# Optimization experiments

Hardware: AMD Instinct MI355X
Metric: run time of the kernel (lower is better)

Reference implementation:

```python
import jax, jax.numpy as jnp
import numpy as np

N, C, T, V = 64, 128, 64, 25   # batch, channels (2*base_channel), frames, joints
MAX_ORDER = 6                  # Adams-Bashforth order used by ODESolver
# _BASHFORTH_COEFFICIENTS[6] / _DIVISOR[6]
_AB_NUM = [4277.0, -7923.0, 9982.0, -7298.0, 2877.0, -475.0]
_AB_DEN = 1440.0


def _init_pe(length, d_model):
    # Sinusoidal positional encoding, shaped [1, d_model, length, 1] like ODEFunc.init_pe
    position = np.arange(length, dtype=np.float32)[:, None]
    div_term = np.exp(np.arange(0, d_model, 2, dtype=np.float32) * -(np.log(10000.0) / d_model))
    pe = np.zeros((length, d_model), dtype=np.float32)
    pe[:, 0::2] = np.sin(position * div_term)
    pe[:, 1::2] = np.cos(position * div_term)
    return jnp.asarray(pe.T[None, :, :, None])


def setup_inputs() -> dict:
    key = jax.random.key(0)
    ks = jax.random.split(key, 8)
    h = jax.random.normal(ks[0], (N, C, T, V), dtype=jnp.float32)
    # replaces torch.rand(B,1,1,1) teacher-forcing draws, one per integration step
    mask_rand = jax.random.uniform(ks[1], (T - MAX_ORDER, N, 1, 1, 1), dtype=jnp.float32)
    # normalized adjacency (row-stochastic-ish), V x V
    A = jax.random.uniform(ks[2], (V, V), dtype=jnp.float32) / V
    pe = _init_pe(3 * T, C)

    def conv_params(k):
        kw, kb = jax.random.split(k)
        s = 1.0 / np.sqrt(C)
        W = jax.random.uniform(kw, (C, C), dtype=jnp.float32, minval=-s, maxval=s)
        b = jax.random.uniform(kb, (C,), dtype=jnp.float32, minval=-s, maxval=s)
        return W, b

    W1, b1 = conv_params(ks[3])
    W2, b2 = conv_params(ks[4])
    W3, b3 = conv_params(ks[5])
    Wp, bp = conv_params(ks[6])
    return dict(h=h, mask_rand=mask_rand, A=A, pe=pe,
                W1=W1, b1=b1, W2=W2, b2=b2, W3=W3, b3=b3, Wp=Wp, bp=bp)


def _ode_func(t, z, A, pe, W1, b1, W2, b2, W3, b3, Wp, bp):
    # z: [N, C, 1, V]; add temporal PE at frame index 3*t
    x = z + jax.lax.dynamic_slice_in_dim(pe, 3 * t, 1, axis=2)

    def gc(x, W, b):
        x = jnp.einsum('vu,nctu->nctv', A, x)                       # graph message passing
        x = jnp.einsum('oc,nctv->notv', W, x) + b[None, :, None, None]  # 1x1 conv
        return jnp.tanh(x)

    x = gc(x, W1, b1)
    x = gc(x, W2, b2)
    x = gc(x, W3, b3)
    return jnp.einsum('oc,nctv->notv', Wp, x) + bp[None, :, None, None]


def _forward(h, mask, A, pe, W1, b1, W2, b2, W3, b3, Wp, bp):
    coeffs = (jnp.asarray(_AB_NUM, dtype=h.dtype) / jnp.asarray(_AB_DEN, dtype=h.dtype))
    ode = lambda t, z: _ode_func(t, z, A, pe, W1, b1, W2, b2, W3, b3, Wp, bp)

    # warm-up: seed the multistep history with observed frames (small fixed loop)
    fs = [ode(t, h[:, :, t:t + 1, :]) for t in range(MAX_ORDER)]
    prev_f = jnp.stack(fs[::-1])                     # [6, N, C, 1, V], most recent first
    z_cand = h[:, :, MAX_ORDER - 1:MAX_ORDER, :]     # zs[5]

    ts = jnp.arange(MAX_ORDER - 1, T - 1)            # t = 5 .. 62
    h_body = jnp.transpose(h[:, :, MAX_ORDER - 1:T - 1, :], (2, 0, 1, 3))[:, :, :, None, :]  # [58,N,C,1,V]

    def step(carry, inp):
        prev_f, z_cand = carry
        t, h_t, m = inp
        z_t = jnp.where(m, z_cand, h_t)              # teacher forcing with prob 0.2
        z_next = z_t + jnp.tensordot(coeffs, prev_f, axes=1)  # Adams-Bashforth update
        f_t = ode(t, z_t)
        prev_f = jnp.concatenate([f_t[None], prev_f[:-1]], axis=0)
        return (prev_f, z_next), z_next

    _, z_outs = jax.lax.scan(step, (prev_f, z_cand), (ts, h_body, mask))
    tail = jnp.transpose(z_outs[:, :, :, 0, :], (1, 2, 0, 3))  # [N, C, 58, V]
    return jnp.concatenate([h[:, :, :MAX_ORDER, :], tail], axis=2)  # [N, C, T, V]


def reference(h, mask_rand, A, pe, W1, b1, W2, b2, W3, b3, Wp, bp):
    return _forward(h, mask_rand < 0.8, A, pe, W1, b1, W2, b2, W3, b3, Wp, bp)
```

## Files before the change

kernel.cpp:

```cpp
#include <hip/hip_runtime.h>

#define NN 64
#define CC 128
#define TT 64
#define VVJ 25
#define FS 28
#define FSLOT 3584

typedef __attribute__((ext_vector_type(4))) float f4;
typedef __attribute__((ext_vector_type(8))) short bh8;
typedef __attribute__((ext_vector_type(4))) short bh4;

#define ZF_OFF   0
#define FT_OFF   14336
#define XUH_OFF  100352
#define XUL_OFF  108544
#define XVH_OFF  116736
#define XVL_OFF  124928
#define LDS_BYTES 133120

__device__ __forceinline__ f4 mfma16(bh8 a, bh8 b, f4 c) {
    return __builtin_amdgcn_mfma_f32_16x16x32_bf16(a, b, c, 0, 0, 0);
}

__device__ __forceinline__ float fast_tanh(float x) {
    float e = __expf(2.f * x);
    return 1.f - 2.f / (e + 1.f);
}

struct HL { short h, l; };
__device__ __forceinline__ HL hilo(float x) {
    unsigned xb = __float_as_uint(x);
    HL r;
    r.h = (short)(xb >> 16);
    float l = x - __uint_as_float(xb & 0xffff0000u);
    r.l = (short)(__float_as_uint(l) >> 16);
    return r;
}

__global__ __launch_bounds__(512, 2)
void infogcn_mfma(const float* __restrict__ h, const float* __restrict__ mr,
                  const float* __restrict__ A, const float* __restrict__ pe,
                  const float* __restrict__ W1, const float* __restrict__ b1,
                  const float* __restrict__ W2, const float* __restrict__ b2,
                  const float* __restrict__ W3, const float* __restrict__ b3,
                  const float* __restrict__ Wp, const float* __restrict__ bp,
                  float* __restrict__ out)
{
    extern __shared__ char lds[];
    float* zf = (float*)(lds + ZF_OFF);
    float* fT = (float*)(lds + FT_OFF);
    char* xUh = lds + XUH_OFF;  char* xUl = lds + XUL_OFF;
    char* xVh = lds + XVH_OFF;  char* xVl = lds + XVL_OFF;

    const int tid  = threadIdx.x;
    const int lane = tid & 63;
    const int w    = tid >> 6;
    const int col  = lane & 15;
    const int kg   = lane >> 4;
    const int n    = blockIdx.x;
    const float* hn = h   + (size_t)n * 204800;
    float*       on = out + (size_t)n * 204800;

    for (int i4 = tid; i4 < LDS_BYTES / 4; i4 += 512) ((unsigned*)lds)[i4] = 0u;
    __syncthreads();

    const int o = 16 * w + col;
    bh8 Wh[4][4], Wl[4][4];
    float bias[4];
    {
        const float* Wm[4] = {W1, W2, W3, Wp};
        const float* Bm[4] = {b1, b2, b3, bp};
        #pragma unroll
        for (int mat = 0; mat < 4; ++mat) {
            bias[mat] = Bm[mat][o];
            #pragma unroll
            for (int ks = 0; ks < 4; ++ks) {
                int c0k = 32 * ks + kg * 8;
                #pragma unroll
                for (int e = 0; e < 8; ++e) {
                    HL t = hilo(Wm[mat][o * CC + c0k + e]);
                    Wh[mat][ks][e] = t.h;
                    Wl[mat][ks][e] = t.l;
                }
            }
        }
    }
    bh8 Ath[2], Atl[2];
    float asum[2];
    #pragma unroll
    for (int nt = 0; nt < 2; ++nt) {
        int v = 16 * nt + col;
        #pragma unroll
        for (int e = 0; e < 8; ++e) {
            int u = kg * 8 + e;
            float x = (v < VVJ && u < VVJ) ? A[v * VVJ + u] : 0.f;
            HL t = hilo(x);
            Ath[nt][e] = t.h;
            Atl[nt][e] = t.l;
        }
        float s = 0.f;
        if (v < VVJ)
            for (int u = 0; u < VVJ; ++u) s += A[v * VVJ + u];
        asum[nt] = s;
    }

    for (int idx = tid; idx < 9600; idx += 512) {
        int c = idx / 75, r2 = idx - c * 75;
        *(float2*)&on[c * 1600 + r2 * 2] = *(const float2*)&hn[c * 1600 + r2 * 2];
    }

    auto amix = [&](bool withPE, int t3) {
        int cA = 16 * w + col;
        int bau = (cA * 64 + kg * 16) ^ ((cA & 7) << 4);
        bh8 xh = *(bh8*)(xUh + bau);
        bh8 xl = *(bh8*)(xUl + bau);
        int c0 = 16 * w + kg * 4;
        float pe4[4];
        if (withPE) {
            #pragma unroll
            for (int i = 0; i < 4; ++i) pe4[i] = pe[(c0 + i) * 192 + t3];
        }
        #pragma unroll
        for (int nt = 0; nt < 2; ++nt) {
            f4 acc;
            if (withPE) {
                #pragma unroll
                for (int i = 0; i < 4; ++i) acc[i] = pe4[i] * asum[nt];
            } else {
                acc = (f4){0.f, 0.f, 0.f, 0.f};
            }
            acc = mfma16(xh, Ath[nt], acc);
            acc = mfma16(xh, Atl[nt], acc);
            acc = mfma16(xl, Ath[nt], acc);
            int v = 16 * nt + col;
            bh4 h4, l4;
            #pragma unroll
            for (int i = 0; i < 4; ++i) {
                HL t = hilo(acc[i]);
                h4[i] = t.h;
                l4[i] = t.l;
            }
            int ba = (v * 256 + c0 * 2) ^ ((v & 7) << 4);
            *(bh4*)(xVh + ba) = h4;
            *(bh4*)(xVl + ba) = l4;
        }
    };

    auto wmix_core = [&](int mat, f4 (&acc)[2], const char* axh, const char* axl) {
        #pragma unroll
        for (int m = 0; m < 2; ++m) {
            int vA = 16 * m + col;
            int sw = (vA & 7) << 4;
            #pragma unroll
            for (int ks = 0; ks < 4; ++ks) {
                int ba = (vA * 256 + ks * 64 + kg * 16) ^ sw;
                bh8 xh = *(bh8*)(axh + ba);
                bh8 xl = *(bh8*)(axl + ba);
                acc[m] = mfma16(xh, Wh[mat][ks], acc[m]);
                acc[m] = mfma16(xh, Wl[mat][ks], acc[m]);
                acc[m] = mfma16(xl, Wh[mat][ks], acc[m]);
            }
        }
    };

    auto gc_store = [&](int mat, const f4 (&acc)[2]) {
        #pragma unroll
        for (int m = 0; m < 2; ++m) {
            int v0 = 16 * m + kg * 4;
            bh4 h4, l4;
            #pragma unroll
            for (int i = 0; i < 4; ++i) {
                float y = fast_tanh(acc[m][i] + bias[mat]);
                HL t = hilo(y);
                h4[i] = t.h;
                l4[i] = t.l;
            }
            int ba = (o * 64 + v0 * 2) ^ ((o & 7) << 4);
            *(bh4*)(xUh + ba) = h4;
            *(bh4*)(xUl + ba) = l4;
        }
    };

    auto gc3_store = [&](const f4 (&acc)[2]) {
        #pragma unroll
        for (int m = 0; m < 2; ++m) {
            #pragma unroll
            for (int i = 0; i < 4; ++i) {
                int v = 16 * m + kg * 4 + i;
                float y = fast_tanh(acc[m][i] + bias[2]);
                HL t = hilo(y);
                int ba = (v * 256 + o * 2) ^ ((v & 7) << 4);
                *(short*)(xUh + ba) = t.h;
                *(short*)(xUl + ba) = t.l;
            }
        }
    };

    auto wp_store = [&](const f4 (&acc)[2], int slot) {
        #pragma unroll
        for (int m = 0; m < 2; ++m) {
            #pragma unroll
            for (int i = 0; i < 4; ++i) {
                int v = 16 * m + kg * 4 + i;
                if (v < VVJ)
                    fT[slot * FSLOT + o * FS + v] = acc[m][i] + bias[3];
            }
        }
    };

    auto ode = [&](int t, int slot) {
        amix(true, 3 * t);
        __syncthreads();
        f4 acc[2];
        acc[0] = acc[1] = (f4){0.f, 0.f, 0.f, 0.f};
        wmix_core(0, acc, xVh, xVl);
        gc_store(0, acc);
        __syncthreads();
        amix(false, 0);
        __syncthreads();
        acc[0] = acc[1] = (f4){0.f, 0.f, 0.f, 0.f};
        wmix_core(1, acc, xVh, xVl);
        gc_store(1, acc);
        __syncthreads();
        amix(false, 0);
        __syncthreads();
        acc[0] = acc[1] = (f4){0.f, 0.f, 0.f, 0.f};
        wmix_core(2, acc, xVh, xVl);
        gc3_store(acc);
        __syncthreads();
        acc[0] = acc[1] = (f4){0.f, 0.f, 0.f, 0.f};
        wmix_core(3, acc, xUh, xUl);
        wp_store(acc, slot);
        __syncthreads();
    };

    #pragma unroll 1
    for (int i = 0; i < 6; ++i) {
        for (int idx = tid; idx < 1024; idx += 512) {
            int vq = idx & 7, c = idx >> 3;
            int v0 = vq * 4;
            int ba = (c * 64 + v0 * 2) ^ ((c & 7) << 4);
            bh4 h4 = (bh4){0,0,0,0}, l4 = (bh4){0,0,0,0};
            if (vq < 7) {
                #pragma unroll
                for (int j = 0; j < 4; ++j) {
                    int v = v0 + j;
                    float z = (v < VVJ) ? hn[c * 1600 + i * 25 + v] : 0.f;
                    HL t = hilo(z);
                    h4[j] = t.h;
                    l4[j] = t.l;
                }
            }
            *(bh4*)(xUh + ba) = h4;
            *(bh4*)(xUl + ba) = l4;
        }
        __syncthreads();
        ode(i, i);
    }

    for (int idx = tid; idx < 1024; idx += 512) {
        int vq = idx & 7, c = idx >> 3;
        if (vq < 7) {
            int v0 = vq * 4;
            #pragma unroll
            for (int j = 0; j < 4; ++j) {
                int v = v0 + j;
                zf[c * FS + v] = (v < VVJ) ? hn[c * 1600 + 125 + v] : 0.f;
            }
        }
    }
    __syncthreads();

    const float coef[6] = { 4277.f/1440.f, -7923.f/1440.f, 9982.f/1440.f,
                            -7298.f/1440.f, 2877.f/1440.f, -475.f/1440.f };
    int head = 5;

    #pragma unroll 1
    for (int t = 5; t < TT - 1; ++t) {
        bool msk = mr[(t - 5) * NN + n] < 0.8f;
        for (int idx = tid; idx < 1024; idx += 512) {
            int vq = idx & 7, c = idx >> 3;
            int v0 = vq * 4;
            int ba = (c * 64 + v0 * 2) ^ ((c & 7) << 4);
            if (vq < 7) {
                f4 zt;
                if (msk) {
                    zt = *(const f4*)&zf[c * FS + v0];
                } else {
                    #pragma unroll
                    for (int j = 0; j < 4; ++j) {
                        int v = v0 + j;
                        zt[j] = (v < VVJ) ? hn[c * 1600 + t * 25 + v] : 0.f;
                    }
                }
                bh4 h4, l4;
                #pragma unroll
                for (int j = 0; j < 4; ++j) {
                    HL tt = hilo(zt[j]);
                    h4[j] = tt.h;
                    l4[j] = tt.l;
                }
                *(bh4*)(xUh + ba) = h4;
                *(bh4*)(xUl + ba) = l4;
                f4 zn = zt;
                #pragma unroll
                for (int k = 0; k < 6; ++k) {
                    int s = head - k; if (s < 0) s += 6;
                    f4 fq = *(const f4*)&fT[s * FSLOT + c * FS + v0];
                    zn += coef[k] * fq;
                }
                *(f4*)&zf[c * FS + v0] = zn;
                #pragma unroll
                for (int j = 0; j < 4; ++j) {
                    int v = v0 + j;
                    if (v < VVJ) on[c * 1600 + (t + 1) * 25 + v] = zn[j];
                }
            } else {
                *(bh4*)(xUh + ba) = (bh4){0,0,0,0};
                *(bh4*)(xUl + ba) = (bh4){0,0,0,0};
            }
        }
        __syncthreads();
        if (t < TT - 2) {
            int slot = head + 1; if (slot >= 6) slot = 0;
            ode(t, slot);
            head = slot;
        }
    }
}

extern "C" void kernel_launch(void* const* d_in, const int* in_sizes, int n_in,
                              void* d_out, int out_size, void* d_ws, size_t ws_size,
                              hipStream_t stream) {
    const float* h  = (const float*)d_in[0];
    const float* mr = (const float*)d_in[1];
    const float* A  = (const float*)d_in[2];
    const float* pe = (const float*)d_in[3];
    const float* W1 = (const float*)d_in[4];
    const float* b1 = (const float*)d_in[5];
    const float* W2 = (const float*)d_in[6];
    const float* b2 = (const float*)d_in[7];
    const float* W3 = (const float*)d_in[8];
    const float* b3 = (const float*)d_in[9];
    const float* Wp = (const float*)d_in[10];
    const float* bp = (const float*)d_in[11];
    float* out = (float*)d_out;

    (void)hipFuncSetAttribute((const void*)infogcn_mfma,
                              hipFuncAttributeMaxDynamicSharedMemorySize, LDS_BYTES);
    infogcn_mfma<<<dim3(NN), dim3(512), LDS_BYTES, stream>>>(
        h, mr, A, pe, W1, b1, W2, b2, W3, b3, Wp, bp, out);
}
```

Measured before the change: 609.8 us.

## Keep ODE state and Adams-Bashforth history in registers, shuffle fragments between stages

The f-history ring buffer and the z state move from LDS into per-thread registers, each laid out in the MFMA output layout. The A-mix input for GC1/GC2 is built with cross-lane shuffles (to_frag) rather than an LDS store and reload. This removes two barriers per ODE evaluation and the LDS traffic of the per-step update, and cuts LDS from about 130KB to 32KB. In exchange, register pressure rises (6x2 f4 history plus the weights) and more shuffles are issued; the constant-index history shift needs full unrolling to stay in registers.

Measured after the change: 528.8 us. 13.3% less time.

```diff
diff --git a/kernel.cpp b/kernel.cpp
--- a/kernel.cpp
+++ b/kernel.cpp
@@ -4,20 +4,16 @@
 #define CC 128
 #define TT 64
 #define VVJ 25
-#define FS 28
-#define FSLOT 3584
 
 typedef __attribute__((ext_vector_type(4))) float f4;
 typedef __attribute__((ext_vector_type(8))) short bh8;
 typedef __attribute__((ext_vector_type(4))) short bh4;
 
-#define ZF_OFF   0
-#define FT_OFF   14336
-#define XUH_OFF  100352
-#define XUL_OFF  108544
-#define XVH_OFF  116736
-#define XVL_OFF  124928
-#define LDS_BYTES 133120
+#define XAH_OFF 0
+#define XAL_OFF 8192
+#define XBH_OFF 16384
+#define XBL_OFF 24576
+#define LDS_BYTES 32768
 
 __device__ __forceinline__ f4 mfma16(bh8 a, bh8 b, f4 c) {
     return __builtin_amdgcn_mfma_f32_16x16x32_bf16(a, b, c, 0, 0, 0);
@@ -39,19 +35,17 @@
 }
 
 __global__ __launch_bounds__(512, 2)
-void infogcn_mfma(const float* __restrict__ h, const float* __restrict__ mr,
-                  const float* __restrict__ A, const float* __restrict__ pe,
-                  const float* __restrict__ W1, const float* __restrict__ b1,
-                  const float* __restrict__ W2, const float* __restrict__ b2,
-                  const float* __restrict__ W3, const float* __restrict__ b3,
-                  const float* __restrict__ Wp, const float* __restrict__ bp,
-                  float* __restrict__ out)
+void infogcn_reg(const float* __restrict__ h, const float* __restrict__ mr,
+                 const float* __restrict__ A, const float* __restrict__ pe,
+                 const float* __restrict__ W1, const float* __restrict__ b1,
+                 const float* __restrict__ W2, const float* __restrict__ b2,
+                 const float* __restrict__ W3, const float* __restrict__ b3,
+                 const float* __restrict__ Wp, const float* __restrict__ bp,
+                 float* __restrict__ out)
 {
     extern __shared__ char lds[];
-    float* zf = (float*)(lds + ZF_OFF);
-    float* fT = (float*)(lds + FT_OFF);
-    char* xUh = lds + XUH_OFF;  char* xUl = lds + XUL_OFF;
-    char* xVh = lds + XVH_OFF;  char* xVl = lds + XVL_OFF;
+    char* xah = lds + XAH_OFF;  char* xal = lds + XAL_OFF;
+    char* xbh = lds + XBH_OFF;  char* xbl = lds + XBL_OFF;
 
     const int tid  = threadIdx.x;
     const int lane = tid & 63;
@@ -61,11 +55,10 @@
     const int n    = blockIdx.x;
     const float* hn = h   + (size_t)n * 204800;
     float*       on = out + (size_t)n * 204800;
+    const int o = 16 * w + col;
 
     for (int i4 = tid; i4 < LDS_BYTES / 4; i4 += 512) ((unsigned*)lds)[i4] = 0u;
-    __syncthreads();
-
-    const int o = 16 * w + col;
+
     bh8 Wh[4][4], Wl[4][4];
     float bias[4];
     {
@@ -79,9 +72,9 @@
                 int c0k = 32 * ks + kg * 8;
                 #pragma unroll
                 for (int e = 0; e < 8; ++e) {
-                    HL t = hilo(Wm[mat][o * CC + c0k + e]);
-                    Wh[mat][ks][e] = t.h;
-                    Wl[mat][ks][e] = t.l;
+                    HL p = hilo(Wm[mat][o * CC + c0k + e]);
+                    Wh[mat][ks][e] = p.h;
+                    Wl[mat][ks][e] = p.l;
                 }
             }
         }
@@ -95,9 +88,9 @@
         for (int e = 0; e < 8; ++e) {
             int u = kg * 8 + e;
             float x = (v < VVJ && u < VVJ) ? A[v * VVJ + u] : 0.f;
-            HL t = hilo(x);
-            Ath[nt][e] = t.h;
-            Atl[nt][e] = t.l;
+            HL p = hilo(x);
+            Ath[nt][e] = p.h;
+            Atl[nt][e] = p.l;
         }
         float s = 0.f;
         if (v < VVJ)
@@ -109,12 +102,9 @@
         int c = idx / 75, r2 = idx - c * 75;
         *(float2*)&on[c * 1600 + r2 * 2] = *(const float2*)&hn[c * 1600 + r2 * 2];
     }
-
-    auto amix = [&](bool withPE, int t3) {
-        int cA = 16 * w + col;
-        int bau = (cA * 64 + kg * 16) ^ ((cA & 7) << 4);
-        bh8 xh = *(bh8*)(xUh + bau);
-        bh8 xl = *(bh8*)(xUl + bau);
+    __syncthreads();
+
+    auto amix_store = [&](bh8 zh, bh8 zl, bool withPE, int t3, char* dh, char* dl) {
         int c0 = 16 * w + kg * 4;
         float pe4[4];
         if (withPE) {
@@ -130,20 +120,20 @@
             } else {
                 acc = (f4){0.f, 0.f, 0.f, 0.f};
             }
-            acc = mfma16(xh, Ath[nt], acc);
-            acc = mfma16(xh, Atl[nt], acc);
-            acc = mfma16(xl, Ath[nt], acc);
+            acc = mfma16(zh, Ath[nt], acc);
+            acc = mfma16(zh, Atl[nt], acc);
+            acc = mfma16(zl, Ath[nt], acc);
             int v = 16 * nt + col;
             bh4 h4, l4;
             #pragma unroll
             for (int i = 0; i < 4; ++i) {
-                HL t = hilo(acc[i]);
-                h4[i] = t.h;
-                l4[i] = t.l;
+                HL p = hilo(acc[i]);
+                h4[i] = p.h;
+                l4[i] = p.l;
             }
             int ba = (v * 256 + c0 * 2) ^ ((v & 7) << 4);
-            *(bh4*)(xVh + ba) = h4;
-            *(bh4*)(xVl + ba) = l4;
+            *(bh4*)(dh + ba) = h4;
+            *(bh4*)(dl + ba) = l4;
         }
     };
 
@@ -164,168 +154,139 @@
         }
     };
 
-    auto gc_store = [&](int mat, const f4 (&acc)[2]) {
-        #pragma unroll
-        for (int m = 0; m < 2; ++m) {
-            int v0 = 16 * m + kg * 4;
-            bh4 h4, l4;
+    auto to_frag = [&](const f4 (&y)[2], bh8& fh, bh8& fl) {
+        #pragma unroll
+        for (int e = 0; e < 8; ++e) {
+            int src = ((((kg & 1) << 1) + (e >> 2)) << 4) + col;
+            float t0 = __shfl(y[0][e & 3], src);
+            float t1 = __shfl(y[1][e & 3], src);
+            float v = (kg < 2) ? t0 : t1;
+            HL p = hilo(v);
+            fh[e] = p.h;
+            fl[e] = p.l;
+        }
+    };
+
+    auto gc3_store = [&](const f4 (&acc)[2], char* dh, char* dl) {
+        #pragma unroll
+        for (int m = 0; m < 2; ++m)
             #pragma unroll
             for (int i = 0; i < 4; ++i) {
-                float y = fast_tanh(acc[m][i] + bias[mat]);
-                HL t = hilo(y);
-                h4[i] = t.h;
-                l4[i] = t.l;
-            }
-            int ba = (o * 64 + v0 * 2) ^ ((o & 7) << 4);
-            *(bh4*)(xUh + ba) = h4;
-            *(bh4*)(xUl + ba) = l4;
-        }
-    };
-
-    auto gc3_store = [&](const f4 (&acc)[2]) {
-        #pragma unroll
-        for (int m = 0; m < 2; ++m) {
-            #pragma unroll
-            for (int i = 0; i < 4; ++i) {
-                int v = 16 * m + kg * 4 + i;
+                int v = 16 * m + 4 * kg + i;
                 float y = fast_tanh(acc[m][i] + bias[2]);
-                HL t = hilo(y);
+                HL p = hilo(y);
                 int ba = (v * 256 + o * 2) ^ ((v & 7) << 4);
-                *(short*)(xUh + ba) = t.h;
-                *(short*)(xUl + ba) = t.l;
-            }
-        }
-    };
-
-    auto wp_store = [&](const f4 (&acc)[2], int slot) {
-        #pragma unroll
-        for (int m = 0; m < 2; ++m) {
-            #pragma unroll
-            for (int i = 0; i < 4; ++i) {
-                int v = 16 * m + kg * 4 + i;
-                if (v < VVJ)
-                    fT[slot * FSLOT + o * FS + v] = acc[m][i] + bias[3];
-            }
-        }
-    };
-
-    auto ode = [&](int t, int slot) {
-        amix(true, 3 * t);
+                *(short*)(dh + ba) = p.h;
+                *(short*)(dl + ba) = p.l;
+            }
+    };
+
+    auto ode = [&](bh8 zh, bh8 zl, int t3, f4 (&fout)[2]) {
+        amix_store(zh, zl, true, t3, xah, xal);
         __syncthreads();
         f4 acc[2];
         acc[0] = acc[1] = (f4){0.f, 0.f, 0.f, 0.f};
-        wmix_core(0, acc, xVh, xVl);
-        gc_store(0, acc);
-        __syncthreads();
-        amix(false, 0);
+        wmix_core(0, acc, xah, xal);
+        {
+            f4 y[2];
+            #pragma unroll
+            for (int m = 0; m < 2; ++m)
+                #pragma unroll
+                for (int i = 0; i < 4; ++i) y[m][i] = fast_tanh(acc[m][i] + bias[0]);
+            bh8 yh, yl;
+            to_frag(y, yh, yl);
+            amix_store(yh, yl, false, 0, xbh, xbl);
+        }
         __syncthreads();
         acc[0] = acc[1] = (f4){0.f, 0.f, 0.f, 0.f};
-        wmix_core(1, acc, xVh, xVl);
-        gc_store(1, acc);
-        __syncthreads();
-        amix(false, 0);
+        wmix_core(1, acc, xbh, xbl);
+        {
+            f4 y[2];
+            #pragma unroll
+            for (int m = 0; m < 2; ++m)
+                #pragma unroll
+                for (int i = 0; i < 4; ++i) y[m][i] = fast_tanh(acc[m][i] + bias[1]);
+            bh8 yh, yl;
+            to_frag(y, yh, yl);
+            amix_store(yh, yl, false, 0, xah, xal);
+        }
         __syncthreads();
         acc[0] = acc[1] = (f4){0.f, 0.f, 0.f, 0.f};
-        wmix_core(2, acc, xVh, xVl);
-        gc3_store(acc);
+        wmix_core(2, acc, xah, xal);
+        gc3_store(acc, xbh, xbl);
         __syncthreads();
         acc[0] = acc[1] = (f4){0.f, 0.f, 0.f, 0.f};
-        wmix_core(3, acc, xUh, xUl);
-        wp_store(acc, slot);
-        __syncthreads();
-    };
-
-    #pragma unroll 1
+        wmix_core(3, acc, xbh, xbl);
+        fout[0] = acc[0] + bias[3];
+        fout[1] = acc[1] + bias[3];
+    };
+
+    f4 fr[6][2];
+    #pragma unroll
     for (int i = 0; i < 6; ++i) {
-        for (int idx = tid; idx < 1024; idx += 512) {
-            int vq = idx & 7, c = idx >> 3;
-            int v0 = vq * 4;
-            int ba = (c * 64 + v0 * 2) ^ ((c & 7) << 4);
-            bh4 h4 = (bh4){0,0,0,0}, l4 = (bh4){0,0,0,0};
-            if (vq < 7) {
-                #pragma unroll
-                for (int j = 0; j < 4; ++j) {
-                    int v = v0 + j;
-                    float z = (v < VVJ) ? hn[c * 1600 + i * 25 + v] : 0.f;
-                    HL t = hilo(z);
-                    h4[j] = t.h;
-                    l4[j] = t.l;
-                }
-            }
-            *(bh4*)(xUh + ba) = h4;
-            *(bh4*)(xUl + ba) = l4;
-        }
-        __syncthreads();
-        ode(i, i);
-    }
-
-    for (int idx = tid; idx < 1024; idx += 512) {
-        int vq = idx & 7, c = idx >> 3;
-        if (vq < 7) {
-            int v0 = vq * 4;
-            #pragma unroll
-            for (int j = 0; j < 4; ++j) {
-                int v = v0 + j;
-                zf[c * FS + v] = (v < VVJ) ? hn[c * 1600 + 125 + v] : 0.f;
-            }
-        }
-    }
-    __syncthreads();
+        bh8 zh, zl;
+        #pragma unroll
+        for (int e = 0; e < 8; ++e) {
+            int u = 8 * kg + e;
+            float zv = (u < VVJ) ? hn[o * 1600 + i * 25 + u] : 0.f;
+            HL p = hilo(zv);
+            zh[e] = p.h;
+            zl[e] = p.l;
+        }
+        ode(zh, zl, 3 * i, fr[5 - i]);
+    }
+
+    f4 zm[2];
+    #pragma unroll
+    for (int m = 0; m < 2; ++m)
+        #pragma unroll
+        for (int i = 0; i < 4; ++i) {
+            int v = 16 * m + 4 * kg + i;
+            zm[m][i] = (v < VVJ) ? hn[o * 1600 + 125 + v] : 0.f;
+        }
 
     const float coef[6] = { 4277.f/1440.f, -7923.f/1440.f, 9982.f/1440.f,
                             -7298.f/1440.f, 2877.f/1440.f, -475.f/1440.f };
-    int head = 5;
 
     #pragma unroll 1
     for (int t = 5; t < TT - 1; ++t) {
         bool msk = mr[(t - 5) * NN + n] < 0.8f;
-        for (int idx = tid; idx < 1024; idx += 512) {
-            int vq = idx & 7, c = idx >> 3;
-            int v0 = vq * 4;
-            int ba = (c * 64 + v0 * 2) ^ ((c & 7) << 4);
-            if (vq < 7) {
-                f4 zt;
-                if (msk) {
-                    zt = *(const f4*)&zf[c * FS + v0];
-                } else {
-                    #pragma unroll
-                    for (int j = 0; j < 4; ++j) {
-                        int v = v0 + j;
-                        zt[j] = (v < VVJ) ? hn[c * 1600 + t * 25 + v] : 0.f;
-                    }
+        f4 zt[2];
+        if (msk) {
+            zt[0] = zm[0]; zt[1] = zm[1];
+        } else {
+            #pragma unroll
+            for (int m = 0; m < 2; ++m)
+                #pragma unroll
+                for (int i = 0; i < 4; ++i) {
+                    int v = 16 * m + 4 * kg + i;
+                    zt[m][i] = (v < VVJ) ? hn[o * 1600 + t * 25 + v] : 0.f;
                 }
-                bh4 h4, l4;
-                #pragma unroll
-                for (int j = 0; j < 4; ++j) {
-                    HL tt = hilo(zt[j]);
-                    h4[j] = tt.h;
-                    l4[j] = tt.l;
-                }
-                *(bh4*)(xUh + ba) = h4;
-                *(bh4*)(xUl + ba) = l4;
-                f4 zn = zt;
-                #pragma unroll
-                for (int k = 0; k < 6; ++k) {
-                    int s = head - k; if (s < 0) s += 6;
-                    f4 fq = *(const f4*)&fT[s * FSLOT + c * FS + v0];
-                    zn += coef[k] * fq;
-                }
-                *(f4*)&zf[c * FS + v0] = zn;
-                #pragma unroll
-                for (int j = 0; j < 4; ++j) {
-                    int v = v0 + j;
-                    if (v < VVJ) on[c * 1600 + (t + 1) * 25 + v] = zn[j];
-                }
-            } else {
-                *(bh4*)(xUh + ba) = (bh4){0,0,0,0};
-                *(bh4*)(xUl + ba) = (bh4){0,0,0,0};
-            }
-        }
-        __syncthreads();
+        }
+        bh8 zh, zl;
+        to_frag(zt, zh, zl);
+        f4 zn[2];
+        #pragma unroll
+        for (int m = 0; m < 2; ++m) {
+            zn[m] = zt[m];
+            #pragma unroll
+            for (int k = 0; k < 6; ++k) zn[m] += coef[k] * fr[k][m];
+        }
+        #pragma unroll
+        for (int m = 0; m < 2; ++m)
+            #pragma unroll
+            for (int i = 0; i < 4; ++i) {
+                int v = 16 * m + 4 * kg + i;
+                if (v < VVJ) on[o * 1600 + (t + 1) * 25 + v] = zn[m][i];
+            }
+        zm[0] = zn[0]; zm[1] = zn[1];
+
         if (t < TT - 2) {
-            int slot = head + 1; if (slot >= 6) slot = 0;
-            ode(t, slot);
-            head = slot;
+            f4 fnew[2];
+            ode(zh, zl, 3 * t, fnew);
+            #pragma unroll
+            for (int k = 5; k > 0; --k) { fr[k][0] = fr[k-1][0]; fr[k][1] = fr[k-1][1]; }
+            fr[0][0] = fnew[0]; fr[0][1] = fnew[1];
         }
     }
 }
@@ -347,8 +308,8 @@
     const float* bp = (const float*)d_in[11];
     float* out = (float*)d_out;
 
-    (void)hipFuncSetAttribute((const void*)infogcn_mfma,
+    (void)hipFuncSetAttribute((const void*)infogcn_reg,
                               hipFuncAttributeMaxDynamicSharedMemorySize, LDS_BYTES);
-    infogcn_mfma<<<dim3(NN), dim3(512), LDS_BYTES, stream>>>(
+    infogcn_reg<<<dim3(NN), dim3(512), LDS_BYTES, stream>>>(
         h, mr, A, pe, W1, b1, W2, b2, W3, b3, Wp, bp, out);
 }
```
